# Optimization experiments

Hardware: AMD Instinct MI355X
Metric: run time of the kernel (lower is better)

The kernel has to match this reference:

```python
import jax, jax.numpy as jnp
import numpy as np

D = 1024        # model dim (== moe_inter_dim, required by Expert's x2*x3)
H = 1024        # expert hidden dim (moe_inter_dim)
E = 8           # n_routed_experts
K = 2           # n_activated_experts (top-k)
I = 2 * 1024    # shared-expert inter dim = n_shared_experts * moe_inter_dim
ROUTE_SCALE = 1.0


def setup_inputs() -> dict:
    key = jax.random.key(0)
    ks = jax.random.split(key, 12)
    s = lambda *sh: 1.0 / np.sqrt(sh[-1])
    return {
        "x":      jax.random.normal(ks[0], (1, 2048, D), jnp.float32),
        "gate_w": jax.random.normal(ks[1], (E, D), jnp.float32) * s(E, D),
        "w1":     jax.random.normal(ks[2], (E, H, D), jnp.float32) * s(H, D),
        "b1":     jax.random.normal(ks[3], (E, H), jnp.float32) * 0.01,
        "w2":     jax.random.normal(ks[4], (E, D, H), jnp.float32) * s(D, H),
        "b2":     jax.random.normal(ks[5], (E, D), jnp.float32) * 0.01,
        "w3":     jax.random.normal(ks[6], (E, H, D), jnp.float32) * s(H, D),
        "b3":     jax.random.normal(ks[7], (E, H), jnp.float32) * 0.01,
        "sw1":    jax.random.normal(ks[8], (I, D), jnp.float32) * s(I, D),
        "sw2":    jax.random.normal(ks[9], (I, D), jnp.float32) * s(I, D),
        "sw3":    jax.random.normal(ks[10], (D, I), jnp.float32) * s(D, I),
    }


def reference(x, gate_w, w1, b1, w2, b2, w3, b3, sw1, sw2, sw3):
    B, S, _ = x.shape
    xt = x.reshape(-1, D)                                  # (T, D)
    # ---- Gate (softmax scoring, n_groups==1, no bias, route_scale=1) ----
    logits = xt @ gate_w.T                                 # (T, E)
    scores = jax.nn.softmax(logits.astype(jnp.float32), axis=-1)
    top_vals, idx = jax.lax.top_k(scores, K)               # (T, K)
    weights = (jnp.take_along_axis(scores, idx, axis=1)
               .astype(x.dtype)) * ROUTE_SCALE             # (T, K)
    # ---- Routed experts: input is scaled by routing weight BEFORE expert ----
    xs = xt[:, None, :] * weights[:, :, None]              # (T, K, D)
    y = jnp.zeros_like(xt)
    for e in range(E):  # fixed small loop over experts (dense masked dispatch)
        mask = (idx == e).astype(x.dtype)                  # (T, K)
        h = jax.nn.silu(jnp.einsum('tkd,hd->tkh', xs, w1[e]) + b1[e])
        x2 = jnp.einsum('tkh,dh->tkd', h, w2[e]) + b2[e]   # (T, K, D)
        x3 = jnp.einsum('tkd,hd->tkh', xs, w3[e]) + b3[e]  # (T, K, H==D)
        y = y + jnp.sum((x2 * x3) * mask[:, :, None], axis=1)
    # ---- Shared experts (SwiGLU MLP, no biases) ----
    z = (jax.nn.silu(xt @ sw1.T) * (xt @ sw2.T)) @ sw3.T   # (T, D)
    return (y + z).reshape(B, S, D)
```

## Files before the change

### kernel.cpp

```cpp
#include <hip/hip_runtime.h>

typedef unsigned short u16;
typedef __attribute__((ext_vector_type(4))) float floatx4;
typedef __attribute__((ext_vector_type(8))) short short8;

#define MAXROWS 5120
#define MAXMT 40

__device__ __forceinline__ u16 f2bf(float f) {
    union { float f; unsigned u; } v; v.f = f;
    unsigned r = v.u + 0x7FFF + ((v.u >> 16) & 1);
    return (u16)(r >> 16);
}
__device__ __forceinline__ float bf2f(u16 h) {
    union { unsigned u; float f; } v; v.u = ((unsigned)h) << 16; return v.f;
}
__device__ __forceinline__ float silu_f(float x) { return x / (1.f + __expf(-x)); }

__device__ __forceinline__ void gl_lds16(const void* g, void* l) {
    __builtin_amdgcn_global_load_lds(
        (__attribute__((address_space(1))) unsigned int*)g,
        (__attribute__((address_space(3))) unsigned int*)l, 16, 0, 0);
}

__device__ __forceinline__ void ld_frags(
    unsigned a0, unsigned a1, unsigned a2, unsigned a3,
    unsigned b0, unsigned b1, unsigned b2, unsigned b3,
    short8& af0, short8& af1, short8& af2, short8& af3,
    short8& bf0, short8& bf1, short8& bf2, short8& bf3) {
    asm volatile(
        "ds_read_b128 %0, %8\n\t"
        "ds_read_b128 %1, %9\n\t"
        "ds_read_b128 %2, %10\n\t"
        "ds_read_b128 %3, %11\n\t"
        "ds_read_b128 %4, %12\n\t"
        "ds_read_b128 %5, %13\n\t"
        "ds_read_b128 %6, %14\n\t"
        "ds_read_b128 %7, %15\n\t"
        "s_waitcnt lgkmcnt(0)"
        : "=&v"(af0), "=&v"(af1), "=&v"(af2), "=&v"(af3),
          "=&v"(bf0), "=&v"(bf1), "=&v"(bf2), "=&v"(bf3)
        : "v"(a0), "v"(a1), "v"(a2), "v"(a3),
          "v"(b0), "v"(b1), "v"(b2), "v"(b3));
}

#define WAIT_VM4() __builtin_amdgcn_s_waitcnt(3956)
#define WAIT_VM0() __builtin_amdgcn_s_waitcnt(3952)
#define BAR()      __builtin_amdgcn_s_barrier()

__global__ void conv_gate(const float* __restrict__ w1, const float* __restrict__ w2,
                          const float* __restrict__ w3, const float* __restrict__ sw1,
                          const float* __restrict__ sw2, const float* __restrict__ sw3,
                          const float* __restrict__ x, const float* __restrict__ gw,
                          u16* __restrict__ W13, u16* __restrict__ W2b,
                          u16* __restrict__ S12, u16* __restrict__ S3b,
                          u16* __restrict__ Xb,
                          int* __restrict__ idxA, float* __restrict__ wA) {
    int bid = blockIdx.x;
    if (bid < 512) {
        int w = threadIdx.x >> 6, lane = threadIdx.x & 63;
        int t = bid * 4 + w;
        const float* xr = x + (size_t)t * 1024;
        float acc[8];
#pragma unroll
        for (int e = 0; e < 8; e++) acc[e] = 0.f;
#pragma unroll
        for (int i = 0; i < 16; i++) {
            float xv = xr[lane + (i << 6)];
#pragma unroll
            for (int e = 0; e < 8; e++) acc[e] += xv * gw[e * 1024 + lane + (i << 6)];
        }
#pragma unroll
        for (int e = 0; e < 8; e++)
            for (int off = 32; off > 0; off >>= 1) acc[e] += __shfl_xor(acc[e], off);
        if (lane == 0) {
            float m = acc[0];
#pragma unroll
            for (int e = 1; e < 8; e++) m = fmaxf(m, acc[e]);
            float p[8], s = 0.f;
#pragma unroll
            for (int e = 0; e < 8; e++) { p[e] = __expf(acc[e] - m); s += p[e]; }
            float inv = 1.f / s;
#pragma unroll
            for (int e = 0; e < 8; e++) p[e] *= inv;
            int i0 = 0;
#pragma unroll
            for (int e = 1; e < 8; e++) if (p[e] > p[i0]) i0 = e;
            int i1 = (i0 == 0) ? 1 : 0;
            for (int e = i1 + 1; e < 8; e++) if (e != i0 && p[e] > p[i1]) i1 = e;
            idxA[2 * t] = i0; idxA[2 * t + 1] = i1;
            wA[2 * t] = p[i0]; wA[2 * t + 1] = p[i1];
        }
        return;
    }
    long j = (long)(bid - 512) * 256 + threadIdx.x;
    const float* src; u16* dst; long d;
    if (j < 2097152) {
        long e = j >> 18; src = w1; dst = W13; d = j + (e << 18);
    } else if ((j -= 2097152) < 2097152) {
        long e = j >> 18; src = w3; dst = W13; d = j + (e << 18) + 262144;
    } else if ((j -= 2097152) < 2097152) { src = w2;  dst = W2b; d = j; }
    else if ((j -= 2097152) < 524288) {
        long rr = j >> 8, c4 = j & 255;
        long br = ((rr >> 4) << 5) + (rr & 15);
        src = sw1; dst = S12; d = (br << 8) + c4;
    } else if ((j -= 524288) < 524288) {
        long rr = j >> 8, c4 = j & 255;
        long br = ((rr >> 4) << 5) + 16 + (rr & 15);
        src = sw2; dst = S12; d = (br << 8) + c4;
    } else if ((j -= 524288) < 524288)     { src = sw3; dst = S3b; d = j; }
    else { j -= 524288; src = x; dst = Xb; d = j; }
    float4 v = ((const float4*)src)[j];
    ushort4 o; o.x = f2bf(v.x); o.y = f2bf(v.y); o.z = f2bf(v.z); o.w = f2bf(v.w);
    ((ushort4*)dst)[d] = o;
}

__global__ void rank_k(const int* __restrict__ idxA, int* __restrict__ tileexp,
                       int* __restrict__ ntiles, int* __restrict__ slot_of) {
    int lane = threadIdx.x;
    const int* my = idxA + lane * 64;
    int h[8];
#pragma unroll
    for (int e = 0; e < 8; e++) h[e] = 0;
    for (int i = 0; i < 64; i++) {
        int v = my[i];
#pragma unroll
        for (int e = 0; e < 8; e++) h[e] += (v == e);
    }
    int excl[8], tot[8];
#pragma unroll
    for (int e = 0; e < 8; e++) {
        int inc = h[e];
        for (int off = 1; off < 64; off <<= 1) {
            int up = __shfl_up(inc, off);
            if (lane >= off) inc += up;
        }
        excl[e] = inc - h[e];
        tot[e] = __shfl(inc, 63);
    }
    int base[8], tiles = 0;
#pragma unroll
    for (int e = 0; e < 8; e++) {
        base[e] = tiles * 128;
        tiles += (tot[e] + 127) >> 7;
    }
    if (lane == 0) {
        ntiles[0] = tiles;
        int t = 0;
        for (int e = 0; e < 8; e++) {
            int te = (tot[e] + 127) >> 7;
            for (int j = 0; j < te; j++) tileexp[t++] = e;
        }
    }
    int c[8];
#pragma unroll
    for (int e = 0; e < 8; e++) c[e] = base[e] + excl[e];
    for (int i = 0; i < 64; i++) {
        int v = my[i], slot = 0;
#pragma unroll
        for (int e = 0; e < 8; e++) slot += (v == e) ? c[e] : 0;
#pragma unroll
        for (int e = 0; e < 8; e++) c[e] += (v == e);
        slot_of[lane * 64 + i] = slot;
    }
}

__global__ void build_xs(const float* __restrict__ x, const float* __restrict__ wA,
                         const int* __restrict__ slot_of, u16* __restrict__ XS) {
    int s = blockIdx.x, i = threadIdx.x;
    int t = s >> 1; float w = wA[s]; int slot = slot_of[s];
    float4 v = ((const float4*)(x + (size_t)t * 1024))[i];
    ushort4 o; o.x = f2bf(v.x * w); o.y = f2bf(v.y * w); o.z = f2bf(v.z * w); o.w = f2bf(v.w * w);
    ((ushort4*)(XS + (size_t)slot * 1024))[i] = o;
}

#define STAGE32(BUF, Ab, Bb, lda, kk)                                          \
    {                                                                          \
        _Pragma("unroll")                                                      \
        for (int t = 0; t < 2; t++) {                                          \
            int r = (w << 4) + (t << 6) + rloc;                                \
            int cg = clds ^ ((r >> 1) & 3);                                    \
            gl_lds16(Ab + (size_t)(m0 + r) * (lda) + (kk) + (cg << 3),         \
                     LDS + (BUF)*4096 + ((w << 4) + (t << 6)) * 32);           \
            gl_lds16(Bb + (size_t)(n0 + r) * (lda) + (kk) + (cg << 3),         \
                     LDS + 8192 + (BUF)*4096 + ((w << 4) + (t << 6)) * 32);    \
        }                                                                      \
    }

#define COMPUTE32(BUF)                                                         \
    {                                                                          \
        short8 af[4], bf[4];                                                   \
        ld_frags(adA[0] + (BUF)*8192, adA[1] + (BUF)*8192,                     \
                 adA[2] + (BUF)*8192, adA[3] + (BUF)*8192,                     \
                 adB[0] + (BUF)*8192, adB[1] + (BUF)*8192,                     \
                 adB[2] + (BUF)*8192, adB[3] + (BUF)*8192,                     \
                 af[0], af[1], af[2], af[3], bf[0], bf[1], bf[2], bf[3]);      \
        _Pragma("unroll")                                                      \
        for (int i = 0; i < 4; i++)                                            \
            _Pragma("unroll")                                                  \
            for (int j = 0; j < 4; j++)                                        \
                acc[i][j] = __builtin_amdgcn_mfma_f32_16x16x32_bf16(           \
                    af[i], bf[j], acc[i][j], 0, 0, 0);                         \
    }

#define KLOOP(NP, Ab, Bb, lda, kbeg)                                           \
    {                                                                          \
        STAGE32(0, Ab, Bb, lda, (kbeg));                                       \
        for (int ii = 0; ii < (NP); ii++) {                                    \
            int kk = (kbeg) + (ii << 6);                                       \
            STAGE32(1, Ab, Bb, lda, kk + 32);                                  \
            WAIT_VM4(); BAR();                                                 \
            COMPUTE32(0);                                                      \
            BAR();                                                             \
            if (ii + 1 < (NP)) {                                               \
                STAGE32(0, Ab, Bb, lda, kk + 64);                              \
                WAIT_VM4();                                                    \
            } else {                                                           \
                WAIT_VM0();                                                    \
            }                                                                  \
            BAR();                                                             \
            COMPUTE32(1);                                                      \
            BAR();                                                             \
        }                                                                      \
    }

#define GEMM_PRE()                                                             \
    int tid = threadIdx.x, w = tid >> 6, lane = tid & 63;                      \
    int wm = w >> 1, wn = w & 1;                                               \
    int rloc = lane >> 2, clds = lane & 3, q = lane >> 4, l15 = lane & 15;     \
    unsigned ldsbase = (unsigned)(size_t)(__attribute__((address_space(3))) u16*)LDS; \
    unsigned adA[4], adB[4];                                                   \
    _Pragma("unroll")                                                          \
    for (int i = 0; i < 4; i++) {                                              \
        int rr = (wm << 6) + (i << 4) + l15;                                   \
        int g = q ^ ((rr >> 1) & 3);                                           \
        adA[i] = ldsbase + rr * 64 + g * 16;                                   \
    }                                                                          \
    _Pragma("unroll")                                                          \
    for (int j = 0; j < 4; j++) {                                              \
        int rr = (wn << 6) + (j << 4) + l15;                                   \
        int g = q ^ ((rr >> 1) & 3);                                           \
        adB[j] = ldsbase + 16384 + rr * 64 + g * 16;                           \
    }                                                                          \
    floatx4 acc[4][4];                                                         \
    _Pragma("unroll")                                                          \
    for (int i = 0; i < 4; i++)                                                \
        _Pragma("unroll")                                                      \
        for (int j = 0; j < 4; j++) {                                          \
            floatx4 z = {0.f, 0.f, 0.f, 0.f}; acc[i][j] = z;                   \
        }

__global__ __launch_bounds__(256) void gemm_A(
    const u16* __restrict__ XS, const u16* __restrict__ Xb,
    const u16* __restrict__ W13, const u16* __restrict__ S12,
    const float* __restrict__ b1, const float* __restrict__ b3,
    u16* __restrict__ H, u16* __restrict__ X3h, u16* __restrict__ G,
    const int* __restrict__ tileexp, const int* __restrict__ ntiles) {
    __shared__ u16 LDS[16384];
    int xcd = blockIdx.x & 7, ws = blockIdx.x >> 3;
    const u16 *Ab, *Bb; int mt, nt, e = 0; bool routed;
    if (ws < 80) {
        routed = true;
        mt = xcd * 5 + (ws >> 4);
        nt = ws & 15;
        if (mt >= ntiles[0]) return;
        e = tileexp[mt];
        Ab = XS; Bb = W13 + ((size_t)e << 21);
    } else {
        routed = false; int s = ws - 80;
        mt = ((xcd >> 2) << 3) + (s >> 3);
        nt = ((xcd & 3) << 3) + (s & 7);
        Ab = Xb; Bb = S12;
    }
    int m0 = mt * 128, n0 = nt * 128;
    GEMM_PRE();

    KLOOP(16, Ab, Bb, 1024, 0);

    if (routed) {
#pragma unroll
        for (int i = 0; i < 4; i++) {
            int rowb = m0 + (wm << 6) + (i << 4) + (q << 2);
#pragma unroll
            for (int j = 0; j < 4; j++) {
                int col = n0 + (wn << 6) + (j << 4) + l15;
#pragma unroll
                for (int r = 0; r < 4; r++) {
                    float v = acc[i][j][r];
                    int rw = rowb + r;
                    if (nt < 8) {
                        H[(size_t)rw * 1024 + col] = f2bf(silu_f(v + b1[e * 1024 + col]));
                    } else {
                        int c2 = col - 1024;
                        X3h[(size_t)rw * 1024 + c2] = f2bf(v + b3[e * 1024 + c2]);
                    }
                }
            }
        }
    } else {
#pragma unroll
        for (int i = 0; i < 4; i++) {
            int rowb = m0 + (wm << 6) + (i << 4) + (q << 2);
#pragma unroll
            for (int jp = 0; jp < 4; jp += 2) {
                int brb = n0 + (wn << 6) + (jp << 4);
                int lcol = ((brb >> 5) << 4) + l15;
#pragma unroll
                for (int r = 0; r < 4; r++) {
                    float u = acc[i][jp][r], v = acc[i][jp + 1][r];
                    G[(size_t)(rowb + r) * 2048 + lcol] = f2bf(silu_f(u) * v);
                }
            }
        }
    }
}

__global__ __launch_bounds__(256) void gemm_B(
    const u16* __restrict__ H, const u16* __restrict__ G,
    const u16* __restrict__ W2b, const u16* __restrict__ S3b,
    const float* __restrict__ b2, const u16* __restrict__ X3h,
    u16* __restrict__ P0, u16* __restrict__ P1,
    float* __restrict__ Z0, float* __restrict__ Z1,
    const int* __restrict__ tileexp, const int* __restrict__ ntiles) {
    __shared__ u16 LDS[16384];
    int xcd = blockIdx.x & 7, ws = blockIdx.x >> 3;
    const u16 *Ab, *Bb; int mt, nt, kc, lda, kbeg, np, e = 0; bool routed;
    if (ws < 80) {
        routed = true;
        mt = xcd * 5 + (ws >> 4);
        int r = ws & 15; nt = r & 7; kc = r >> 3;
        if (mt >= ntiles[0]) return;
        e = tileexp[mt];
        Ab = H; Bb = W2b + ((size_t)e << 20); lda = 1024; kbeg = kc << 9; np = 8;
    } else {
        routed = false; int s = ws - 80;
        kc = s & 1; int s2 = s >> 1;
        mt = ((xcd >> 1) << 2) + (s2 >> 2);
        nt = ((xcd & 1) << 2) + (s2 & 3);
        Ab = G; Bb = S3b; lda = 2048; kbeg = kc << 10; np = 16;
    }
    int m0 = mt * 128, n0 = nt * 128;
    GEMM_PRE();

    KLOOP(np, Ab, Bb, lda, kbeg);

    if (routed) {
        u16* Pk = kc ? P1 : P0;
#pragma unroll
        for (int i = 0; i < 4; i++) {
            int rowb = m0 + (wm << 6) + (i << 4) + (q << 2);
#pragma unroll
            for (int j = 0; j < 4; j++) {
                int col = n0 + (wn << 6) + (j << 4) + l15;
#pragma unroll
                for (int r = 0; r < 4; r++) {
                    int rw = rowb + r;
                    float v = acc[i][j][r] + (kc == 0 ? b2[e * 1024 + col] : 0.f);
                    float pv = v * bf2f(X3h[(size_t)rw * 1024 + col]);
                    Pk[(size_t)rw * 1024 + col] = f2bf(pv);
                }
            }
        }
    } else {
        float* Zk = kc ? Z1 : Z0;
#pragma unroll
        for (int i = 0; i < 4; i++) {
            int rowb = m0 + (wm << 6) + (i << 4) + (q << 2);
#pragma unroll
            for (int j = 0; j < 4; j++) {
                int col = n0 + (wn << 6) + (j << 4) + l15;
#pragma unroll
                for (int r = 0; r < 4; r++)
                    Zk[(size_t)(rowb + r) * 1024 + col] = acc[i][j][r];
            }
        }
    }
}

__global__ void final_k(const float* __restrict__ Z0, const float* __restrict__ Z1,
                        const u16* __restrict__ P0, const u16* __restrict__ P1,
                        const int* __restrict__ slot_of, float* __restrict__ out) {
    int i = blockIdx.x * 256 + threadIdx.x;
    int t = i >> 8, c4 = i & 255;
    int s0 = slot_of[2 * t], s1 = slot_of[2 * t + 1];
    float4 z0 = ((const float4*)Z0)[(size_t)t * 256 + c4];
    float4 z1 = ((const float4*)Z1)[(size_t)t * 256 + c4];
    ushort4 a0 = ((const ushort4*)P0)[(size_t)s0 * 256 + c4];
    ushort4 a1 = ((const ushort4*)P1)[(size_t)s0 * 256 + c4];
    ushort4 c0 = ((const ushort4*)P0)[(size_t)s1 * 256 + c4];
    ushort4 c1 = ((const ushort4*)P1)[(size_t)s1 * 256 + c4];
    float4 o;
    o.x = z0.x + z1.x + bf2f(a0.x) + bf2f(a1.x) + bf2f(c0.x) + bf2f(c1.x);
    o.y = z0.y + z1.y + bf2f(a0.y) + bf2f(a1.y) + bf2f(c0.y) + bf2f(c1.y);
    o.z = z0.z + z1.z + bf2f(a0.z) + bf2f(a1.z) + bf2f(c0.z) + bf2f(c1.z);
    o.w = z0.w + z1.w + bf2f(a0.w) + bf2f(a1.w) + bf2f(c0.w) + bf2f(c1.w);
    ((float4*)out)[(size_t)t * 256 + c4] = o;
}

extern "C" void kernel_launch(void* const* d_in, const int* in_sizes, int n_in,
                              void* d_out, int out_size, void* d_ws, size_t ws_size,
                              hipStream_t stream) {
    const float* x   = (const float*)d_in[0];
    const float* gw  = (const float*)d_in[1];
    const float* w1  = (const float*)d_in[2];
    const float* b1  = (const float*)d_in[3];
    const float* w2  = (const float*)d_in[4];
    const float* b2  = (const float*)d_in[5];
    const float* w3  = (const float*)d_in[6];
    const float* b3  = (const float*)d_in[7];
    const float* sw1 = (const float*)d_in[8];
    const float* sw2 = (const float*)d_in[9];
    const float* sw3 = (const float*)d_in[10];
    float* out = (float*)d_out;

    char* p = (char*)d_ws;
    int* ntiles  = (int*)(p + 192);
    int* tileexp = (int*)(p + 256);
    size_t off = 4096;
    u16*   XS      = (u16*)(p + off);   off += (size_t)MAXROWS * 1024 * 2;
    int*   idxA    = (int*)(p + off);   off += 16384;
    float* wA      = (float*)(p + off); off += 16384;
    int*   slot_of = (int*)(p + off);   off += 16384;
    u16*   H       = (u16*)(p + off);   off += (size_t)MAXROWS * 1024 * 2;
    u16*   X3h     = (u16*)(p + off);   off += (size_t)MAXROWS * 1024 * 2;
    u16*   P0      = (u16*)(p + off);   off += (size_t)MAXROWS * 1024 * 2;
    u16*   P1      = (u16*)(p + off);   off += (size_t)MAXROWS * 1024 * 2;
    float* Z0      = (float*)(p + off); off += (size_t)2048 * 1024 * 4;
    float* Z1      = (float*)(p + off); off += (size_t)2048 * 1024 * 4;
    u16*   W13     = (u16*)(p + off);   off += (size_t)8 * 2048 * 1024 * 2;
    u16*   W2b     = (u16*)(p + off);   off += (size_t)8 * 1024 * 1024 * 2;
    u16*   S12     = (u16*)(p + off);   off += (size_t)4096 * 1024 * 2;
    u16*   S3b     = (u16*)(p + off);   off += (size_t)1024 * 2048 * 2;
    u16*   Xb      = (u16*)(p + off);   off += (size_t)2048 * 1024 * 2;
    u16*   G       = (u16*)(p + off);   off += (size_t)2048 * 2048 * 2;

    conv_gate<<<33280, 256, 0, stream>>>(w1, w2, w3, sw1, sw2, sw3, x, gw,
                                         W13, W2b, S12, S3b, Xb, idxA, wA);
    rank_k<<<1, 64, 0, stream>>>(idxA, tileexp, ntiles, slot_of);
    build_xs<<<4096, 256, 0, stream>>>(x, wA, slot_of, XS);

    gemm_A<<<1152, 256, 0, stream>>>(XS, Xb, W13, S12, b1, b3, H, X3h, G,
                                     tileexp, ntiles);
    gemm_B<<<896, 256, 0, stream>>>(H, G, W2b, S3b, b2, X3h, P0, P1, Z0, Z1,
                                    tileexp, ntiles);
    final_k<<<2048, 256, 0, stream>>>(Z0, Z1, P0, P1, slot_of, out);
}
```

Baseline: 313.2 us.

## Triple-buffer GEMM K-loop and overlap W2/SW3 bf16 conversion with gemm_A

After: 308.9 us. No clear change (-1.4%).

```diff
diff --git a/kernel.cpp b/kernel.cpp
--- a/kernel.cpp
+++ b/kernel.cpp
@@ -44,16 +44,15 @@
           "v"(b0), "v"(b1), "v"(b2), "v"(b3));
 }
 
+#define WAIT_VM8() __builtin_amdgcn_s_waitcnt(3960)
 #define WAIT_VM4() __builtin_amdgcn_s_waitcnt(3956)
 #define WAIT_VM0() __builtin_amdgcn_s_waitcnt(3952)
 #define BAR()      __builtin_amdgcn_s_barrier()
 
-__global__ void conv_gate(const float* __restrict__ w1, const float* __restrict__ w2,
-                          const float* __restrict__ w3, const float* __restrict__ sw1,
-                          const float* __restrict__ sw2, const float* __restrict__ sw3,
+__global__ void conv_gate(const float* __restrict__ w1, const float* __restrict__ w3,
+                          const float* __restrict__ sw1, const float* __restrict__ sw2,
                           const float* __restrict__ x, const float* __restrict__ gw,
-                          u16* __restrict__ W13, u16* __restrict__ W2b,
-                          u16* __restrict__ S12, u16* __restrict__ S3b,
+                          u16* __restrict__ W13, u16* __restrict__ S12,
                           u16* __restrict__ Xb,
                           int* __restrict__ idxA, float* __restrict__ wA) {
     int bid = blockIdx.x;
@@ -99,8 +98,7 @@
         long e = j >> 18; src = w1; dst = W13; d = j + (e << 18);
     } else if ((j -= 2097152) < 2097152) {
         long e = j >> 18; src = w3; dst = W13; d = j + (e << 18) + 262144;
-    } else if ((j -= 2097152) < 2097152) { src = w2;  dst = W2b; d = j; }
-    else if ((j -= 2097152) < 524288) {
+    } else if ((j -= 2097152) < 524288) {
         long rr = j >> 8, c4 = j & 255;
         long br = ((rr >> 4) << 5) + (rr & 15);
         src = sw1; dst = S12; d = (br << 8) + c4;
@@ -108,8 +106,7 @@
         long rr = j >> 8, c4 = j & 255;
         long br = ((rr >> 4) << 5) + 16 + (rr & 15);
         src = sw2; dst = S12; d = (br << 8) + c4;
-    } else if ((j -= 524288) < 524288)     { src = sw3; dst = S3b; d = j; }
-    else { j -= 524288; src = x; dst = Xb; d = j; }
+    } else { j -= 524288; src = x; dst = Xb; d = j; }
     float4 v = ((const float4*)src)[j];
     ushort4 o; o.x = f2bf(v.x); o.y = f2bf(v.y); o.z = f2bf(v.z); o.w = f2bf(v.w);
     ((ushort4*)dst)[d] = o;
@@ -181,19 +178,18 @@
             int r = (w << 4) + (t << 6) + rloc;                                \
             int cg = clds ^ ((r >> 1) & 3);                                    \
             gl_lds16(Ab + (size_t)(m0 + r) * (lda) + (kk) + (cg << 3),         \
-                     LDS + (BUF)*4096 + ((w << 4) + (t << 6)) * 32);           \
+                     LDS + (BUF) * 4096 + ((w << 4) + (t << 6)) * 32);         \
             gl_lds16(Bb + (size_t)(n0 + r) * (lda) + (kk) + (cg << 3),         \
-                     LDS + 8192 + (BUF)*4096 + ((w << 4) + (t << 6)) * 32);    \
+                     LDS + 12288 + (BUF) * 4096 + ((w << 4) + (t << 6)) * 32); \
         }                                                                      \
     }
 
 #define COMPUTE32(BUF)                                                         \
     {                                                                          \
+        unsigned bo = (unsigned)(BUF) << 13;                                   \
         short8 af[4], bf[4];                                                   \
-        ld_frags(adA[0] + (BUF)*8192, adA[1] + (BUF)*8192,                     \
-                 adA[2] + (BUF)*8192, adA[3] + (BUF)*8192,                     \
-                 adB[0] + (BUF)*8192, adB[1] + (BUF)*8192,                     \
-                 adB[2] + (BUF)*8192, adB[3] + (BUF)*8192,                     \
+        ld_frags(adA[0] + bo, adA[1] + bo, adA[2] + bo, adA[3] + bo,           \
+                 adB[0] + bo, adB[1] + bo, adB[2] + bo, adB[3] + bo,           \
                  af[0], af[1], af[2], af[3], bf[0], bf[1], bf[2], bf[3]);      \
         _Pragma("unroll")                                                      \
         for (int i = 0; i < 4; i++)                                            \
@@ -203,25 +199,23 @@
                     af[i], bf[j], acc[i][j], 0, 0, 0);                         \
     }
 
-#define KLOOP(NP, Ab, Bb, lda, kbeg)                                           \
+#define KLOOP3(NSTEP, Ab, Bb, lda, kbeg)                                       \
     {                                                                          \
         STAGE32(0, Ab, Bb, lda, (kbeg));                                       \
-        for (int ii = 0; ii < (NP); ii++) {                                    \
-            int kk = (kbeg) + (ii << 6);                                       \
-            STAGE32(1, Ab, Bb, lda, kk + 32);                                  \
-            WAIT_VM4(); BAR();                                                 \
-            COMPUTE32(0);                                                      \
+        STAGE32(1, Ab, Bb, lda, (kbeg) + 32);                                  \
+        int cb = 0, nb = 1, sb = 2;                                            \
+        for (int ii = 0; ii + 2 < (NSTEP); ii++) {                             \
+            STAGE32(sb, Ab, Bb, lda, (kbeg) + ((ii + 2) << 5));                \
+            WAIT_VM8(); BAR();                                                 \
+            COMPUTE32(cb);                                                     \
             BAR();                                                             \
-            if (ii + 1 < (NP)) {                                               \
-                STAGE32(0, Ab, Bb, lda, kk + 64);                              \
-                WAIT_VM4();                                                    \
-            } else {                                                           \
-                WAIT_VM0();                                                    \
-            }                                                                  \
-            BAR();                                                             \
-            COMPUTE32(1);                                                      \
-            BAR();                                                             \
+            int tt = cb; cb = nb; nb = sb; sb = tt;                            \
         }                                                                      \
+        WAIT_VM4(); BAR();                                                     \
+        COMPUTE32(cb);                                                         \
+        BAR();                                                                 \
+        WAIT_VM0(); BAR();                                                     \
+        COMPUTE32(nb);                                                         \
     }
 
 #define GEMM_PRE()                                                             \
@@ -240,7 +234,7 @@
     for (int j = 0; j < 4; j++) {                                              \
         int rr = (wn << 6) + (j << 4) + l15;                                   \
         int g = q ^ ((rr >> 1) & 3);                                           \
-        adB[j] = ldsbase + 16384 + rr * 64 + g * 16;                           \
+        adB[j] = ldsbase + 24576 + rr * 64 + g * 16;                           \
     }                                                                          \
     floatx4 acc[4][4];                                                         \
     _Pragma("unroll")                                                          \
@@ -255,9 +249,26 @@
     const u16* __restrict__ W13, const u16* __restrict__ S12,
     const float* __restrict__ b1, const float* __restrict__ b3,
     u16* __restrict__ H, u16* __restrict__ X3h, u16* __restrict__ G,
-    const int* __restrict__ tileexp, const int* __restrict__ ntiles) {
-    __shared__ u16 LDS[16384];
-    int xcd = blockIdx.x & 7, ws = blockIdx.x >> 3;
+    const int* __restrict__ tileexp, const int* __restrict__ ntiles,
+    const float* __restrict__ w2f, const float* __restrict__ sw3f,
+    u16* __restrict__ W2b, u16* __restrict__ S3b) {
+    __shared__ u16 LDS[24576];
+    int bid = blockIdx.x;
+    if (bid >= 1152) {
+        long j0 = (long)(bid - 1152) * 256 + threadIdx.x;
+#pragma unroll
+        for (int it = 0; it < 5; it++) {
+            long j = j0 + (long)it * 524288;
+            const float* src; u16* dst; long d = j;
+            if (j < 2097152) { src = w2f; dst = W2b; }
+            else             { d = j - 2097152; src = sw3f; dst = S3b; }
+            float4 v = ((const float4*)src)[d];
+            ushort4 o; o.x = f2bf(v.x); o.y = f2bf(v.y); o.z = f2bf(v.z); o.w = f2bf(v.w);
+            ((ushort4*)dst)[d] = o;
+        }
+        return;
+    }
+    int xcd = bid & 7, ws = bid >> 3;
     const u16 *Ab, *Bb; int mt, nt, e = 0; bool routed;
     if (ws < 80) {
         routed = true;
@@ -275,7 +286,7 @@
     int m0 = mt * 128, n0 = nt * 128;
     GEMM_PRE();
 
-    KLOOP(16, Ab, Bb, 1024, 0);
+    KLOOP3(32, Ab, Bb, 1024, 0);
 
     if (routed) {
 #pragma unroll
@@ -322,27 +333,27 @@
     u16* __restrict__ P0, u16* __restrict__ P1,
     float* __restrict__ Z0, float* __restrict__ Z1,
     const int* __restrict__ tileexp, const int* __restrict__ ntiles) {
-    __shared__ u16 LDS[16384];
+    __shared__ u16 LDS[24576];
     int xcd = blockIdx.x & 7, ws = blockIdx.x >> 3;
-    const u16 *Ab, *Bb; int mt, nt, kc, lda, kbeg, np, e = 0; bool routed;
+    const u16 *Ab, *Bb; int mt, nt, kc, lda, kbeg, nstep, e = 0; bool routed;
     if (ws < 80) {
         routed = true;
         mt = xcd * 5 + (ws >> 4);
         int r = ws & 15; nt = r & 7; kc = r >> 3;
         if (mt >= ntiles[0]) return;
         e = tileexp[mt];
-        Ab = H; Bb = W2b + ((size_t)e << 20); lda = 1024; kbeg = kc << 9; np = 8;
+        Ab = H; Bb = W2b + ((size_t)e << 20); lda = 1024; kbeg = kc << 9; nstep = 16;
     } else {
         routed = false; int s = ws - 80;
         kc = s & 1; int s2 = s >> 1;
         mt = ((xcd >> 1) << 2) + (s2 >> 2);
         nt = ((xcd & 1) << 2) + (s2 & 3);
-        Ab = G; Bb = S3b; lda = 2048; kbeg = kc << 10; np = 16;
+        Ab = G; Bb = S3b; lda = 2048; kbeg = kc << 10; nstep = 32;
     }
     int m0 = mt * 128, n0 = nt * 128;
     GEMM_PRE();
 
-    KLOOP(np, Ab, Bb, lda, kbeg);
+    KLOOP3(nstep, Ab, Bb, lda, kbeg);
 
     if (routed) {
         u16* Pk = kc ? P1 : P0;
@@ -434,13 +445,13 @@
     u16*   Xb      = (u16*)(p + off);   off += (size_t)2048 * 1024 * 2;
     u16*   G       = (u16*)(p + off);   off += (size_t)2048 * 2048 * 2;
 
-    conv_gate<<<33280, 256, 0, stream>>>(w1, w2, w3, sw1, sw2, sw3, x, gw,
-                                         W13, W2b, S12, S3b, Xb, idxA, wA);
+    conv_gate<<<23040, 256, 0, stream>>>(w1, w3, sw1, sw2, x, gw,
+                                         W13, S12, Xb, idxA, wA);
     rank_k<<<1, 64, 0, stream>>>(idxA, tileexp, ntiles, slot_of);
     build_xs<<<4096, 256, 0, stream>>>(x, wA, slot_of, XS);
 
-    gemm_A<<<1152, 256, 0, stream>>>(XS, Xb, W13, S12, b1, b3, H, X3h, G,
-                                     tileexp, ntiles);
+    gemm_A<<<3200, 256, 0, stream>>>(XS, Xb, W13, S12, b1, b3, H, X3h, G,
+                                     tileexp, ntiles, w2, sw3, W2b, S3b);
     gemm_B<<<896, 256, 0, stream>>>(H, G, W2b, S3b, b2, X3h, P0, P1, Z0, Z1,
                                     tileexp, ntiles);
     final_k<<<2048, 256, 0, stream>>>(Z0, Z1, P0, P1, slot_of, out);
```

## Enlarge GEMM tiles to 256x256 with 4-stage LDS pipeline and 8 waves

Applied to the files above, without the earlier changes.

After: 309.0 us. No clear change (-1.3%).

```diff
diff --git a/kernel.cpp b/kernel.cpp
--- a/kernel.cpp
+++ b/kernel.cpp
@@ -5,7 +5,6 @@
 typedef __attribute__((ext_vector_type(8))) short short8;
 
 #define MAXROWS 5120
-#define MAXMT 40
 
 __device__ __forceinline__ u16 f2bf(float f) {
     union { float f; unsigned u; } v; v.f = f;
@@ -44,6 +43,20 @@
           "v"(b0), "v"(b1), "v"(b2), "v"(b3));
 }
 
+__device__ __forceinline__ void ld_frags4(
+    unsigned a0, unsigned a1, unsigned a2, unsigned a3,
+    short8& f0, short8& f1, short8& f2, short8& f3) {
+    asm volatile(
+        "ds_read_b128 %0, %4\n\t"
+        "ds_read_b128 %1, %5\n\t"
+        "ds_read_b128 %2, %6\n\t"
+        "ds_read_b128 %3, %7\n\t"
+        "s_waitcnt lgkmcnt(0)"
+        : "=&v"(f0), "=&v"(f1), "=&v"(f2), "=&v"(f3)
+        : "v"(a0), "v"(a1), "v"(a2), "v"(a3));
+}
+
+#define WAIT_VM8() __builtin_amdgcn_s_waitcnt(3960)
 #define WAIT_VM4() __builtin_amdgcn_s_waitcnt(3956)
 #define WAIT_VM0() __builtin_amdgcn_s_waitcnt(3952)
 #define BAR()      __builtin_amdgcn_s_barrier()
@@ -116,6 +129,7 @@
 }
 
 __global__ void rank_k(const int* __restrict__ idxA, int* __restrict__ tileexp,
+                       int* __restrict__ tilem0, int* __restrict__ tilevalid,
                        int* __restrict__ ntiles, int* __restrict__ slot_of) {
     int lane = threadIdx.x;
     const int* my = idxA + lane * 64;
@@ -145,12 +159,17 @@
         tiles += (tot[e] + 127) >> 7;
     }
     if (lane == 0) {
-        ntiles[0] = tiles;
-        int t = 0;
+        int t256 = 0;
         for (int e = 0; e < 8; e++) {
-            int te = (tot[e] + 127) >> 7;
-            for (int j = 0; j < te; j++) tileexp[t++] = e;
-        }
+            int t128 = (tot[e] + 127) >> 7;
+            for (int j = 0; j < t128; j += 2) {
+                tileexp[t256] = e;
+                tilem0[t256] = base[e] + (j << 7);
+                tilevalid[t256] = ((t128 - j) >= 2) ? 256 : 128;
+                t256++;
+            }
+        }
+        ntiles[0] = t256;
     }
     int c[8];
 #pragma unroll
@@ -174,65 +193,68 @@
     ((ushort4*)(XS + (size_t)slot * 1024))[i] = o;
 }
 
-#define STAGE32(BUF, Ab, Bb, lda, kk)                                          \
+#define STAGE_PAIR(Ab, Bb, lda, kbeg, TT, RND)                                 \
     {                                                                          \
+        int r_ = (w << 4) + ((RND) << 7) + rloc;                               \
+        int cg_ = clds ^ ((r_ >> 1) & 3);                                      \
+        int kk_ = (kbeg) + ((TT) << 5);                                        \
+        int db_ = (((TT) & 3) << 14) + (((w << 4) + ((RND) << 7)) << 5);       \
+        gl_lds16((Ab) + (size_t)(m0 + r_) * (lda) + kk_ + (cg_ << 3),          \
+                 LDS + db_);                                                   \
+        gl_lds16((Bb) + (size_t)(n0 + r_) * (lda) + kk_ + (cg_ << 3),          \
+                 LDS + 8192 + db_);                                            \
+    }
+
+#define MFMA4(AF, IOFF)                                                        \
+    _Pragma("unroll")                                                          \
+    for (int i_ = 0; i_ < 4; i_++)                                             \
         _Pragma("unroll")                                                      \
-        for (int t = 0; t < 2; t++) {                                          \
-            int r = (w << 4) + (t << 6) + rloc;                                \
-            int cg = clds ^ ((r >> 1) & 3);                                    \
-            gl_lds16(Ab + (size_t)(m0 + r) * (lda) + (kk) + (cg << 3),         \
-                     LDS + (BUF)*4096 + ((w << 4) + (t << 6)) * 32);           \
-            gl_lds16(Bb + (size_t)(n0 + r) * (lda) + (kk) + (cg << 3),         \
-                     LDS + 8192 + (BUF)*4096 + ((w << 4) + (t << 6)) * 32);    \
-        }                                                                      \
-    }
-
-#define COMPUTE32(BUF)                                                         \
+        for (int j_ = 0; j_ < 4; j_++)                                         \
+            acc[i_ + (IOFF)][j_] = __builtin_amdgcn_mfma_f32_16x16x32_bf16(    \
+                AF[i_], bf[j_], acc[i_ + (IOFF)][j_], 0, 0, 0);
+
+#define KLOOP(NSTEP, Ab, Bb, lda, kbeg)                                        \
     {                                                                          \
-        short8 af[4], bf[4];                                                   \
-        ld_frags(adA[0] + (BUF)*8192, adA[1] + (BUF)*8192,                     \
-                 adA[2] + (BUF)*8192, adA[3] + (BUF)*8192,                     \
-                 adB[0] + (BUF)*8192, adB[1] + (BUF)*8192,                     \
-                 adB[2] + (BUF)*8192, adB[3] + (BUF)*8192,                     \
-                 af[0], af[1], af[2], af[3], bf[0], bf[1], bf[2], bf[3]);      \
-        _Pragma("unroll")                                                      \
-        for (int i = 0; i < 4; i++)                                            \
-            _Pragma("unroll")                                                  \
-            for (int j = 0; j < 4; j++)                                        \
-                acc[i][j] = __builtin_amdgcn_mfma_f32_16x16x32_bf16(           \
-                    af[i], bf[j], acc[i][j], 0, 0, 0);                         \
-    }
-
-#define KLOOP(NP, Ab, Bb, lda, kbeg)                                           \
-    {                                                                          \
-        STAGE32(0, Ab, Bb, lda, (kbeg));                                       \
-        for (int ii = 0; ii < (NP); ii++) {                                    \
-            int kk = (kbeg) + (ii << 6);                                       \
-            STAGE32(1, Ab, Bb, lda, kk + 32);                                  \
-            WAIT_VM4(); BAR();                                                 \
-            COMPUTE32(0);                                                      \
-            BAR();                                                             \
-            if (ii + 1 < (NP)) {                                               \
-                STAGE32(0, Ab, Bb, lda, kk + 64);                              \
-                WAIT_VM4();                                                    \
-            } else {                                                           \
-                WAIT_VM0();                                                    \
+        STAGE_PAIR(Ab, Bb, lda, kbeg, 0, 0); STAGE_PAIR(Ab, Bb, lda, kbeg, 0, 1); \
+        STAGE_PAIR(Ab, Bb, lda, kbeg, 1, 0); STAGE_PAIR(Ab, Bb, lda, kbeg, 1, 1); \
+        STAGE_PAIR(Ab, Bb, lda, kbeg, 2, 0); STAGE_PAIR(Ab, Bb, lda, kbeg, 2, 1); \
+        WAIT_VM8(); BAR();                                                     \
+        for (int t = 0; t < (NSTEP); t++) {                                    \
+            unsigned bo = (unsigned)(t & 3) << 15;                             \
+            bool more = (t + 3 < (NSTEP));                                     \
+            if (more) STAGE_PAIR(Ab, Bb, lda, kbeg, t + 3, 0);                 \
+            short8 af[4], bf[4], a2[4];                                        \
+            ld_frags(adA[0] + bo, adA[1] + bo, adA[2] + bo, adA[3] + bo,       \
+                     adB[0] + bo, adB[1] + bo, adB[2] + bo, adB[3] + bo,       \
+                     af[0], af[1], af[2], af[3], bf[0], bf[1], bf[2], bf[3]);  \
+            __builtin_amdgcn_s_setprio(1);                                     \
+            MFMA4(af, 0);                                                      \
+            __builtin_amdgcn_s_setprio(0);                                     \
+            if (more) STAGE_PAIR(Ab, Bb, lda, kbeg, t + 3, 1);                 \
+            ld_frags4(adA[4] + bo, adA[5] + bo, adA[6] + bo, adA[7] + bo,      \
+                      a2[0], a2[1], a2[2], a2[3]);                             \
+            if (t < (NSTEP) - 1) {                                             \
+                int rem = (NSTEP) - 1 - t;                                     \
+                if (rem >= 3) WAIT_VM8();                                      \
+                else if (rem == 2) WAIT_VM4();                                 \
+                else WAIT_VM0();                                               \
+                BAR();                                                         \
             }                                                                  \
-            BAR();                                                             \
-            COMPUTE32(1);                                                      \
-            BAR();                                                             \
+            __builtin_amdgcn_s_setprio(1);                                     \
+            MFMA4(a2, 4);                                                      \
+            __builtin_amdgcn_s_setprio(0);                                     \
         }                                                                      \
     }
 
 #define GEMM_PRE()                                                             \
     int tid = threadIdx.x, w = tid >> 6, lane = tid & 63;                      \
-    int wm = w >> 1, wn = w & 1;                                               \
+    int wm = w >> 2, wn = w & 3;                                               \
     int rloc = lane >> 2, clds = lane & 3, q = lane >> 4, l15 = lane & 15;     \
     unsigned ldsbase = (unsigned)(size_t)(__attribute__((address_space(3))) u16*)LDS; \
-    unsigned adA[4], adB[4];                                                   \
+    unsigned adA[8], adB[4];                                                   \
     _Pragma("unroll")                                                          \
-    for (int i = 0; i < 4; i++) {                                              \
-        int rr = (wm << 6) + (i << 4) + l15;                                   \
+    for (int i = 0; i < 8; i++) {                                              \
+        int rr = (wm << 7) + (i << 4) + l15;                                   \
         int g = q ^ ((rr >> 1) & 3);                                           \
         adA[i] = ldsbase + rr * 64 + g * 16;                                   \
     }                                                                          \
@@ -242,45 +264,46 @@
         int g = q ^ ((rr >> 1) & 3);                                           \
         adB[j] = ldsbase + 16384 + rr * 64 + g * 16;                           \
     }                                                                          \
-    floatx4 acc[4][4];                                                         \
+    floatx4 acc[8][4];                                                         \
     _Pragma("unroll")                                                          \
-    for (int i = 0; i < 4; i++)                                                \
+    for (int i = 0; i < 8; i++)                                                \
         _Pragma("unroll")                                                      \
         for (int j = 0; j < 4; j++) {                                          \
             floatx4 z = {0.f, 0.f, 0.f, 0.f}; acc[i][j] = z;                   \
         }
 
-__global__ __launch_bounds__(256) void gemm_A(
+__global__ __launch_bounds__(512, 2) void gemm_A(
     const u16* __restrict__ XS, const u16* __restrict__ Xb,
     const u16* __restrict__ W13, const u16* __restrict__ S12,
     const float* __restrict__ b1, const float* __restrict__ b3,
     u16* __restrict__ H, u16* __restrict__ X3h, u16* __restrict__ G,
-    const int* __restrict__ tileexp, const int* __restrict__ ntiles) {
-    __shared__ u16 LDS[16384];
+    const int* __restrict__ tileexp, const int* __restrict__ tilem0,
+    const int* __restrict__ tilevalid, const int* __restrict__ ntiles) {
+    __shared__ u16 LDS[65536];
     int xcd = blockIdx.x & 7, ws = blockIdx.x >> 3;
-    const u16 *Ab, *Bb; int mt, nt, e = 0; bool routed;
-    if (ws < 80) {
+    const u16 *Ab, *Bb; int m0, n0, nt = 0, e = 0, vcnt = 256; bool routed;
+    if (ws < 24) {
         routed = true;
-        mt = xcd * 5 + (ws >> 4);
-        nt = ws & 15;
+        int mt = xcd * 3 + (ws >> 3);
+        nt = ws & 7;
         if (mt >= ntiles[0]) return;
-        e = tileexp[mt];
+        e = tileexp[mt]; m0 = tilem0[mt]; vcnt = tilevalid[mt];
+        n0 = nt * 256;
         Ab = XS; Bb = W13 + ((size_t)e << 21);
     } else {
-        routed = false; int s = ws - 80;
-        mt = ((xcd >> 2) << 3) + (s >> 3);
-        nt = ((xcd & 3) << 3) + (s & 7);
+        routed = false; int s = ws - 24;
+        m0 = xcd * 256; n0 = s * 256;
         Ab = Xb; Bb = S12;
     }
-    int m0 = mt * 128, n0 = nt * 128;
     GEMM_PRE();
 
-    KLOOP(16, Ab, Bb, 1024, 0);
+    KLOOP(32, Ab, Bb, 1024, 0);
 
     if (routed) {
 #pragma unroll
-        for (int i = 0; i < 4; i++) {
-            int rowb = m0 + (wm << 6) + (i << 4) + (q << 2);
+        for (int i = 0; i < 8; i++) {
+            if (((wm << 7) + (i << 4)) >= vcnt) continue;
+            int rowb = m0 + (wm << 7) + (i << 4) + (q << 2);
 #pragma unroll
             for (int j = 0; j < 4; j++) {
                 int col = n0 + (wn << 6) + (j << 4) + l15;
@@ -288,7 +311,7 @@
                 for (int r = 0; r < 4; r++) {
                     float v = acc[i][j][r];
                     int rw = rowb + r;
-                    if (nt < 8) {
+                    if (nt < 4) {
                         H[(size_t)rw * 1024 + col] = f2bf(silu_f(v + b1[e * 1024 + col]));
                     } else {
                         int c2 = col - 1024;
@@ -299,8 +322,8 @@
         }
     } else {
 #pragma unroll
-        for (int i = 0; i < 4; i++) {
-            int rowb = m0 + (wm << 6) + (i << 4) + (q << 2);
+        for (int i = 0; i < 8; i++) {
+            int rowb = m0 + (wm << 7) + (i << 4) + (q << 2);
 #pragma unroll
             for (int jp = 0; jp < 4; jp += 2) {
                 int brb = n0 + (wn << 6) + (jp << 4);
@@ -315,40 +338,40 @@
     }
 }
 
-__global__ __launch_bounds__(256) void gemm_B(
+__global__ __launch_bounds__(512, 2) void gemm_B(
     const u16* __restrict__ H, const u16* __restrict__ G,
     const u16* __restrict__ W2b, const u16* __restrict__ S3b,
     const float* __restrict__ b2, const u16* __restrict__ X3h,
-    u16* __restrict__ P0, u16* __restrict__ P1,
-    float* __restrict__ Z0, float* __restrict__ Z1,
-    const int* __restrict__ tileexp, const int* __restrict__ ntiles) {
-    __shared__ u16 LDS[16384];
+    u16* __restrict__ P0, u16* __restrict__ P1, float* __restrict__ Z,
+    const int* __restrict__ tileexp, const int* __restrict__ tilem0,
+    const int* __restrict__ tilevalid, const int* __restrict__ ntiles) {
+    __shared__ u16 LDS[65536];
     int xcd = blockIdx.x & 7, ws = blockIdx.x >> 3;
-    const u16 *Ab, *Bb; int mt, nt, kc, lda, kbeg, np, e = 0; bool routed;
-    if (ws < 80) {
+    const u16 *Ab, *Bb; int m0, n0, kc, kbeg, lda, e = 0, vcnt = 256; bool routed;
+    if (ws < 24) {
         routed = true;
-        mt = xcd * 5 + (ws >> 4);
-        int r = ws & 15; nt = r & 7; kc = r >> 3;
+        int mt = xcd * 3 + (ws >> 3);
+        int r = ws & 7; int nt = r & 3; kc = r >> 2;
         if (mt >= ntiles[0]) return;
-        e = tileexp[mt];
-        Ab = H; Bb = W2b + ((size_t)e << 20); lda = 1024; kbeg = kc << 9; np = 8;
+        e = tileexp[mt]; m0 = tilem0[mt]; vcnt = tilevalid[mt];
+        n0 = nt * 256;
+        Ab = H; Bb = W2b + ((size_t)e << 20); lda = 1024; kbeg = kc << 9;
     } else {
-        routed = false; int s = ws - 80;
-        kc = s & 1; int s2 = s >> 1;
-        mt = ((xcd >> 1) << 2) + (s2 >> 2);
-        nt = ((xcd & 1) << 2) + (s2 & 3);
-        Ab = G; Bb = S3b; lda = 2048; kbeg = kc << 10; np = 16;
-    }
-    int m0 = mt * 128, n0 = nt * 128;
+        routed = false; int s = ws - 24;
+        kc = s >> 2; int nt = s & 3;
+        m0 = xcd * 256; n0 = nt * 256;
+        Ab = G; Bb = S3b; lda = 2048; kbeg = kc << 9;
+    }
     GEMM_PRE();
 
-    KLOOP(np, Ab, Bb, lda, kbeg);
+    KLOOP(16, Ab, Bb, lda, kbeg);
 
     if (routed) {
         u16* Pk = kc ? P1 : P0;
 #pragma unroll
-        for (int i = 0; i < 4; i++) {
-            int rowb = m0 + (wm << 6) + (i << 4) + (q << 2);
+        for (int i = 0; i < 8; i++) {
+            if (((wm << 7) + (i << 4)) >= vcnt) continue;
+            int rowb = m0 + (wm << 7) + (i << 4) + (q << 2);
 #pragma unroll
             for (int j = 0; j < 4; j++) {
                 int col = n0 + (wn << 6) + (j << 4) + l15;
@@ -362,10 +385,10 @@
             }
         }
     } else {
-        float* Zk = kc ? Z1 : Z0;
-#pragma unroll
-        for (int i = 0; i < 4; i++) {
-            int rowb = m0 + (wm << 6) + (i << 4) + (q << 2);
+        float* Zk = Z + (size_t)kc * 2097152;
+#pragma unroll
+        for (int i = 0; i < 8; i++) {
+            int rowb = m0 + (wm << 7) + (i << 4) + (q << 2);
 #pragma unroll
             for (int j = 0; j < 4; j++) {
                 int col = n0 + (wn << 6) + (j << 4) + l15;
@@ -377,23 +400,26 @@
     }
 }
 
-__global__ void final_k(const float* __restrict__ Z0, const float* __restrict__ Z1,
+__global__ void final_k(const float* __restrict__ Z,
                         const u16* __restrict__ P0, const u16* __restrict__ P1,
                         const int* __restrict__ slot_of, float* __restrict__ out) {
     int i = blockIdx.x * 256 + threadIdx.x;
     int t = i >> 8, c4 = i & 255;
     int s0 = slot_of[2 * t], s1 = slot_of[2 * t + 1];
-    float4 z0 = ((const float4*)Z0)[(size_t)t * 256 + c4];
-    float4 z1 = ((const float4*)Z1)[(size_t)t * 256 + c4];
+    size_t zi = (size_t)t * 256 + c4;
+    float4 z0 = ((const float4*)Z)[zi];
+    float4 z1 = ((const float4*)(Z + 2097152))[zi];
+    float4 z2 = ((const float4*)(Z + 4194304))[zi];
+    float4 z3 = ((const float4*)(Z + 6291456))[zi];
     ushort4 a0 = ((const ushort4*)P0)[(size_t)s0 * 256 + c4];
     ushort4 a1 = ((const ushort4*)P1)[(size_t)s0 * 256 + c4];
     ushort4 c0 = ((const ushort4*)P0)[(size_t)s1 * 256 + c4];
     ushort4 c1 = ((const ushort4*)P1)[(size_t)s1 * 256 + c4];
     float4 o;
-    o.x = z0.x + z1.x + bf2f(a0.x) + bf2f(a1.x) + bf2f(c0.x) + bf2f(c1.x);
-    o.y = z0.y + z1.y + bf2f(a0.y) + bf2f(a1.y) + bf2f(c0.y) + bf2f(c1.y);
-    o.z = z0.z + z1.z + bf2f(a0.z) + bf2f(a1.z) + bf2f(c0.z) + bf2f(c1.z);
-    o.w = z0.w + z1.w + bf2f(a0.w) + bf2f(a1.w) + bf2f(c0.w) + bf2f(c1.w);
+    o.x = z0.x + z1.x + z2.x + z3.x + bf2f(a0.x) + bf2f(a1.x) + bf2f(c0.x) + bf2f(c1.x);
+    o.y = z0.y + z1.y + z2.y + z3.y + bf2f(a0.y) + bf2f(a1.y) + bf2f(c0.y) + bf2f(c1.y);
+    o.z = z0.z + z1.z + z2.z + z3.z + bf2f(a0.z) + bf2f(a1.z) + bf2f(c0.z) + bf2f(c1.z);
+    o.w = z0.w + z1.w + z2.w + z3.w + bf2f(a0.w) + bf2f(a1.w) + bf2f(c0.w) + bf2f(c1.w);
     ((float4*)out)[(size_t)t * 256 + c4] = o;
 }
 
@@ -414,8 +440,10 @@
     float* out = (float*)d_out;
 
     char* p = (char*)d_ws;
-    int* ntiles  = (int*)(p + 192);
-    int* tileexp = (int*)(p + 256);
+    int* ntiles    = (int*)(p + 192);
+    int* tileexp   = (int*)(p + 256);
+    int* tilem0    = (int*)(p + 512);
+    int* tilevalid = (int*)(p + 768);
     size_t off = 4096;
     u16*   XS      = (u16*)(p + off);   off += (size_t)MAXROWS * 1024 * 2;
     int*   idxA    = (int*)(p + off);   off += 16384;
@@ -425,8 +453,7 @@
     u16*   X3h     = (u16*)(p + off);   off += (size_t)MAXROWS * 1024 * 2;
     u16*   P0      = (u16*)(p + off);   off += (size_t)MAXROWS * 1024 * 2;
     u16*   P1      = (u16*)(p + off);   off += (size_t)MAXROWS * 1024 * 2;
-    float* Z0      = (float*)(p + off); off += (size_t)2048 * 1024 * 4;
-    float* Z1      = (float*)(p + off); off += (size_t)2048 * 1024 * 4;
+    float* Z       = (float*)(p + off); off += (size_t)4 * 2048 * 1024 * 4;
     u16*   W13     = (u16*)(p + off);   off += (size_t)8 * 2048 * 1024 * 2;
     u16*   W2b     = (u16*)(p + off);   off += (size_t)8 * 1024 * 1024 * 2;
     u16*   S12     = (u16*)(p + off);   off += (size_t)4096 * 1024 * 2;
@@ -436,12 +463,12 @@
 
     conv_gate<<<33280, 256, 0, stream>>>(w1, w2, w3, sw1, sw2, sw3, x, gw,
                                          W13, W2b, S12, S3b, Xb, idxA, wA);
-    rank_k<<<1, 64, 0, stream>>>(idxA, tileexp, ntiles, slot_of);
+    rank_k<<<1, 64, 0, stream>>>(idxA, tileexp, tilem0, tilevalid, ntiles, slot_of);
     build_xs<<<4096, 256, 0, stream>>>(x, wA, slot_of, XS);
 
-    gemm_A<<<1152, 256, 0, stream>>>(XS, Xb, W13, S12, b1, b3, H, X3h, G,
-                                     tileexp, ntiles);
-    gemm_B<<<896, 256, 0, stream>>>(H, G, W2b, S3b, b2, X3h, P0, P1, Z0, Z1,
-                                    tileexp, ntiles);
-    final_k<<<2048, 256, 0, stream>>>(Z0, Z1, P0, P1, slot_of, out);
-}
+    gemm_A<<<320, 512, 0, stream>>>(XS, Xb, W13, S12, b1, b3, H, X3h, G,
+                                    tileexp, tilem0, tilevalid, ntiles);
+    gemm_B<<<320, 512, 0, stream>>>(H, G, W2b, S3b, b2, X3h, P0, P1, Z,
+                                    tileexp, tilem0, tilevalid, ntiles);
+    final_k<<<2048, 256, 0, stream>>>(Z, P0, P1, slot_of, out);
+}
```
